# Optimization experiments

Hardware: AMD Instinct MI355X
Metric: run time of the kernel (lower is better)

## Reference

```python
import jax, jax.numpy as jnp
import numpy as np

NG, NL, NCAM, NP, ED = 8, 4, 6, 7, 256  # groups, levels, cams, key points, embed dims
GD = ED // NG
FIX_SCALE = jnp.array([[0.0, 0.0, 0.0], [0.45, 0.0, 0.0], [-0.45, 0.0, 0.0],
                       [0.0, 0.45, 0.0], [0.0, -0.45, 0.0], [0.0, 0.0, 0.45],
                       [0.0, 0.0, -0.45]], dtype=jnp.float32)


def grid_sample_bilinear(feat, grid):
    """feat [N,C,H,W], grid [N,A,P,2] in [-1,1]; bilinear, zeros padding, align_corners=False."""
    N, C, H, W = feat.shape
    A, P = grid.shape[1], grid.shape[2]
    gx = (grid[..., 0] + 1.0) * (W * 0.5) - 0.5
    gy = (grid[..., 1] + 1.0) * (H * 0.5) - 0.5
    x0 = jnp.floor(gx)
    y0 = jnp.floor(gy)
    wx1 = gx - x0
    wy1 = gy - y0
    feat_flat = feat.reshape(N, C, H * W)

    def gather(xi, yi, w):
        valid = (xi >= 0) & (xi <= W - 1) & (yi >= 0) & (yi <= H - 1)
        xc = jnp.clip(xi, 0, W - 1).astype(jnp.int32)
        yc = jnp.clip(yi, 0, H - 1).astype(jnp.int32)
        idx = (yc * W + xc).reshape(N, 1, A * P)
        vals = jnp.take_along_axis(feat_flat, idx, axis=2)  # [N,C,A*P]
        return vals * (w * valid).reshape(N, 1, A * P)

    out = (gather(x0, y0, (1.0 - wx1) * (1.0 - wy1))
           + gather(x0 + 1.0, y0, wx1 * (1.0 - wy1))
           + gather(x0, y0 + 1.0, (1.0 - wx1) * wy1)
           + gather(x0 + 1.0, y0 + 1.0, wx1 * wy1))
    return out.reshape(N, C, A, P)


def _forward(instance_feature, anchor, anchor_embed, feat0, feat1, feat2, feat3,
             projection_mat, image_wh, w_fc, b_fc, w_out, b_out):
    B, A = anchor.shape[:2]
    # --- key point generation (box_code_size=8: size + yaw rotation + translation) ---
    size = jnp.exp(anchor[..., 3:6])[:, :, None, :]           # [B,A,1,3]
    kp = FIX_SCALE * size                                      # [B,A,7,3]
    sin, cos = anchor[..., 6], anchor[..., 7]
    z = jnp.zeros_like(cos)
    o = jnp.ones_like(cos)
    rot = jnp.stack([jnp.stack([cos, -sin, z], -1),
                     jnp.stack([sin, cos, z], -1),
                     jnp.stack([z, z, o], -1)], -2)            # [B,A,3,3]
    kp = jnp.einsum('baij,bapj->bapi', rot, kp) + anchor[..., None, 0:3]

    # --- attention weights: softmax over cams*levels*pts per group ---
    feature = instance_feature + anchor_embed
    w = feature @ w_fc.T + b_fc                                # [B,A,NG*NCAM*NL*NP]
    w = jax.nn.softmax(w.reshape(B, A, NCAM * NL * NP, NG), axis=2)
    w = w.reshape(B, A, NCAM, NL, NP, NG)

    # --- project key points to normalized image coords ---
    pts = jnp.concatenate([kp, jnp.ones_like(kp[..., :1])], -1)  # [B,A,7,4]
    p2d = jnp.einsum('bcij,bapj->bcapi', projection_mat, pts)[..., :3]
    xy = p2d[..., :2] / jnp.maximum(p2d[..., 2:3], 1e-5)
    xy = xy / jnp.maximum(image_wh[:, :, None, None], 1e-5)
    grid = (xy * 2.0 - 1.0).reshape(B * NCAM, A, NP, 2)

    # --- multilevel bilinear sampling ---
    levels = [feat0, feat1, feat2, feat3]
    sampled = jnp.stack([grid_sample_bilinear(f.reshape((B * NCAM,) + f.shape[2:]), grid)
                         for f in levels], axis=1)             # [B*Ncam,NL,C,A,P]
    feats = sampled.reshape(B, NCAM, NL, ED, A, NP).transpose(0, 4, 1, 2, 5, 3)  # [B,A,Ncam,NL,P,C]
    feats = feats.reshape(B, A, NCAM, NL, NP, NG, GD)

    # --- weighted fusion over cams, levels, then sum over key points ---
    fused = jnp.einsum('bacnpgd,bacnpg->bagd', feats, w).reshape(B, A, ED)
    return fused @ w_out.T + b_out


def setup_inputs() -> dict:
    ks = jax.random.split(jax.random.key(0), 13)
    B, A = 2, 900
    return {
        'instance_feature': jax.random.normal(ks[0], (B, A, ED), jnp.float32),
        'anchor': jax.random.normal(ks[1], (B, A, 8), jnp.float32),
        'anchor_embed': jax.random.normal(ks[2], (B, A, ED), jnp.float32),
        'feat0': jax.random.normal(ks[3], (B, NCAM, ED, 64, 176), jnp.float32),
        'feat1': jax.random.normal(ks[4], (B, NCAM, ED, 32, 88), jnp.float32),
        'feat2': jax.random.normal(ks[5], (B, NCAM, ED, 16, 44), jnp.float32),
        'feat3': jax.random.normal(ks[6], (B, NCAM, ED, 8, 22), jnp.float32),
        'projection_mat': jax.random.normal(ks[7], (B, NCAM, 4, 4), jnp.float32),
        'image_wh': jnp.ones((B, NCAM, 2), jnp.float32),
        'w_fc': jax.random.normal(ks[8], (NG * NCAM * NL * NP, ED), jnp.float32) * 0.02,
        'b_fc': jax.random.normal(ks[9], (NG * NCAM * NL * NP,), jnp.float32) * 0.02,
        'w_out': jax.random.normal(ks[10], (ED, ED), jnp.float32) * 0.02,
        'b_out': jax.random.normal(ks[11], (ED,), jnp.float32) * 0.02,
    }


def reference(instance_feature, anchor, anchor_embed, feat0, feat1, feat2, feat3,
              projection_mat, image_wh, w_fc, b_fc, w_out, b_out):
    return _forward(instance_feature, anchor, anchor_embed, feat0, feat1, feat2, feat3,
                    projection_mat, image_wh, w_fc, b_fc, w_out, b_out)
```

## Files before the change

kernel.cpp:

```cpp
#include <hip/hip_runtime.h>
#include <math.h>

constexpr int B = 2, A = 900, ED = 256, NG = 8, NCAM = 6, NL = 4, NP = 7;
constexpr int NJ = NG * NCAM * NL * NP;
constexpr int NBA = B * A;
constexpr int NE = NCAM * NL * NP;

__constant__ float FIXS[NP][3] = {
  {0.f,0.f,0.f},{0.45f,0.f,0.f},{-0.45f,0.f,0.f},
  {0.f,0.45f,0.f},{0.f,-0.45f,0.f},{0.f,0.f,0.45f},{0.f,0.f,-0.45f}};

__constant__ int cH[NL]  = {64,32,16,8};
__constant__ int cW[NL]  = {176,88,44,22};
__constant__ int cHW[NL] = {11264,2816,704,176};

__global__ __launch_bounds__(256) void k_tr(const float* __restrict__ in,
                                            float* __restrict__ out, int R, int C)
{
  __shared__ float tile[32][33];
  const int r0 = blockIdx.y * 32, c0 = blockIdx.x * 32;
  const int tx = threadIdx.x, ty = threadIdx.y;
#pragma unroll
  for (int kk = 0; kk < 4; ++kk) {
    const int r = r0 + ty + kk*8, c = c0 + tx;
    if (r < R && c < C) tile[ty + kk*8][tx] = in[(size_t)r*C + c];
  }
  __syncthreads();
#pragma unroll
  for (int kk = 0; kk < 4; ++kk) {
    const int c = c0 + ty + kk*8, r = r0 + tx;
    if (r < R && c < C) out[(size_t)c*R + r] = tile[tx][ty + kk*8];
  }
}

__global__ __launch_bounds__(192) void k_fc(const float* __restrict__ inst,
    const float* __restrict__ emb, const float* __restrict__ wt,
    const float* __restrict__ b_fc, float* __restrict__ wraw)
{
  __shared__ float fsh[8][ED];
  const int a0 = blockIdx.x * 8;
  const int j  = blockIdx.y * 192 + threadIdx.x;
  const int t  = threadIdx.x;

  for (int i = t; i < 8 * ED; i += 192) {
    const int a = i >> 8, k = i & 255;
    const size_t idx = (size_t)(a0 + a) * ED + k;
    fsh[a][k] = inst[idx] + emb[idx];
  }
  __syncthreads();

  float acc[8] = {0.f,0.f,0.f,0.f,0.f,0.f,0.f,0.f};
  for (int k = 0; k < ED; k += 4) {
    float w0 = wt[(size_t)(k+0)*NJ + j];
    float w1 = wt[(size_t)(k+1)*NJ + j];
    float w2 = wt[(size_t)(k+2)*NJ + j];
    float w3 = wt[(size_t)(k+3)*NJ + j];
#pragma unroll
    for (int a = 0; a < 8; ++a)
      acc[a] += w0*fsh[a][k] + w1*fsh[a][k+1] + w2*fsh[a][k+2] + w3*fsh[a][k+3];
  }
  const float bj = b_fc[j];
#pragma unroll
  for (int a = 0; a < 8; ++a)
    wraw[(size_t)(a0+a)*NJ + j] = acc[a] + bj;
}

__global__ __launch_bounds__(256) void k_sample_g(
    const float* __restrict__ anchor, const float* __restrict__ proj,
    const float* __restrict__ wh, const float* __restrict__ wraw,
    const float* __restrict__ f0, const float* __restrict__ f1,
    const float* __restrict__ f2, const float* __restrict__ f3,
    float* __restrict__ fused)
{
  __shared__ float wsh[NJ];
  __shared__ float gridsh[NCAM][NP][2];
  __shared__ const float* cbase[NE];
  __shared__ float4 cwt[NE];
  __shared__ int4   cmeta[NE];
  __shared__ int wcnt[4];

  const int ba = blockIdx.x;
  const int b  = ba / A;
  const int t  = threadIdx.x;

  for (int j = t; j < NJ; j += 256) wsh[j] = wraw[(size_t)ba*NJ + j];

  if (t < NCAM*NP) {
    const int c = t / NP, p = t % NP;
    const float* an = anchor + (size_t)ba * 8;
    const float sx = expf(an[3]), sy = expf(an[4]), sz = expf(an[5]);
    const float sn = an[6], cs = an[7];
    const float kx = FIXS[p][0]*sx, ky = FIXS[p][1]*sy, kz = FIXS[p][2]*sz;
    const float px = cs*kx - sn*ky + an[0];
    const float py = sn*kx + cs*ky + an[1];
    const float pz = kz + an[2];
    const float* P = proj + ((size_t)(b*NCAM + c))*16;
    const float X = P[0]*px + P[1]*py + P[2]*pz  + P[3];
    const float Y = P[4]*px + P[5]*py + P[6]*pz  + P[7];
    const float Z = P[8]*px + P[9]*py + P[10]*pz + P[11];
    const float zc  = fmaxf(Z, 1e-5f);
    const float whx = fmaxf(wh[(b*NCAM+c)*2+0], 1e-5f);
    const float why = fmaxf(wh[(b*NCAM+c)*2+1], 1e-5f);
    gridsh[c][p][0] = (X/zc/whx)*2.f - 1.f;
    gridsh[c][p][1] = (Y/zc/why)*2.f - 1.f;
  }
  __syncthreads();

  bool valid = false;
  int fl = 0, Wl = 0, HWl = 0;
  float wx1 = 0.f, wy1 = 0.f;
  const float* bptr = nullptr;
  if (t < NE) {
    const int c = t / (NL*NP); const int r = t % (NL*NP);
    const int l = r / NP, p = r % NP;
    Wl = cW[l]; HWl = cHW[l];
    const int Hl = cH[l];
    const float gx = (gridsh[c][p][0] + 1.f) * (Wl * 0.5f) - 0.5f;
    const float gy = (gridsh[c][p][1] + 1.f) * (Hl * 0.5f) - 0.5f;
    const float x0f = floorf(gx), y0f = floorf(gy);
    const bool vx0 = (x0f >=  0.f) & (x0f <= (float)(Wl-1));
    const bool vx1 = (x0f >= -1.f) & (x0f <= (float)(Wl-2));
    const bool vy0 = (y0f >=  0.f) & (y0f <= (float)(Hl-1));
    const bool vy1 = (y0f >= -1.f) & (y0f <= (float)(Hl-2));
    fl = ((vx0&&vy0)?1:0) | ((vx1&&vy0)?2:0) | ((vx0&&vy1)?4:0) | ((vx1&&vy1)?8:0);
    if (fl) {
      wx1 = gx - x0f; wy1 = gy - y0f;
      const int x0 = (int)x0f, y0 = (int)y0f;
      const float* fp = (l==0) ? f0 : (l==1) ? f1 : (l==2) ? f2 : f3;
      bptr = fp + (size_t)(b*NCAM + c) * ED * HWl + (long long)(y0*Wl + x0);
      valid = true;
    }
  }

  const unsigned long long mask = __ballot(valid);
  const int lane = t & 63, wv = t >> 6;
  if (lane == 0) wcnt[wv] = __popcll(mask);
  __syncthreads();
  int off = 0, nv = 0;
#pragma unroll
  for (int i = 0; i < 4; ++i) { if (i < wv) off += wcnt[i]; nv += wcnt[i]; }
  if (valid) {
    const int pos = off + __popcll(mask & ((1ull << lane) - 1ull));
    cbase[pos] = bptr;
    cwt[pos]   = make_float4((1.f-wx1)*(1.f-wy1), wx1*(1.f-wy1),
                             (1.f-wx1)*wy1,       wx1*wy1);
    cmeta[pos] = make_int4(Wl, HWl, fl, t);
  }

  {
    const int g = t >> 5, ln = t & 31;
    float m = -3.4e38f;
    for (int i = ln; i < NE; i += 32) m = fmaxf(m, wsh[i*NG + g]);
#pragma unroll
    for (int mk = 16; mk >= 1; mk >>= 1) m = fmaxf(m, __shfl_xor(m, mk));
    float s = 0.f;
    for (int i = ln; i < NE; i += 32) {
      const float e = expf(wsh[i*NG + g] - m);
      wsh[i*NG + g] = e;
      s += e;
    }
#pragma unroll
    for (int mk = 16; mk >= 1; mk >>= 1) s += __shfl_xor(s, mk);
    const float inv = 1.f / s;
    for (int i = ln; i < NE; i += 32) wsh[i*NG + g] *= inv;
  }
  __syncthreads();

  float acc = 0.f;
  const int g = t >> 5;
  for (int i = 0; i < nv; ++i) {
    const float* bp = cbase[i];
    const float4 w4 = cwt[i];
    const int4 m = cmeta[i];
    const float* pb = bp + (long long)t * m.y;
    const float aw = wsh[m.w*NG + g];
    float sv = 0.f;
    const int f = m.z;
    if (f == 15) {
      sv = w4.x*pb[0] + w4.y*pb[1] + w4.z*pb[m.x] + w4.w*pb[m.x+1];
    } else {
      if (f & 1) sv += w4.x*pb[0];
      if (f & 2) sv += w4.y*pb[1];
      if (f & 4) sv += w4.z*pb[m.x];
      if (f & 8) sv += w4.w*pb[m.x+1];
    }
    acc += aw * sv;
  }
  fused[(size_t)ba*ED + t] = acc;
}

__global__ __launch_bounds__(256) void k_out(const float* __restrict__ fused,
    const float* __restrict__ w_out, const float* __restrict__ b_out,
    float* __restrict__ out)
{
  __shared__ float fsh[8][ED];
  const int a0 = blockIdx.x * 8;
  const int t = threadIdx.x;
#pragma unroll
  for (int k = 0; k < 8; ++k) fsh[k][t] = fused[(size_t)(a0+k)*ED + t];
  __syncthreads();
  float acc[8] = {0.f,0.f,0.f,0.f,0.f,0.f,0.f,0.f};
  for (int i = 0; i < ED; i += 4) {
    const float4 w4 = *(const float4*)&w_out[(size_t)t*ED + i];
#pragma unroll
    for (int k = 0; k < 8; ++k) {
      const float4 fv = *(const float4*)&fsh[k][i];
      acc[k] += w4.x*fv.x + w4.y*fv.y + w4.z*fv.z + w4.w*fv.w;
    }
  }
  const float bo = b_out[t];
#pragma unroll
  for (int k = 0; k < 8; ++k) out[(size_t)(a0+k)*ED + t] = acc[k] + bo;
}

extern "C" void kernel_launch(void* const* d_in, const int* in_sizes, int n_in,
                              void* d_out, int out_size, void* d_ws, size_t ws_size,
                              hipStream_t stream) {
  const float* inst   = (const float*)d_in[0];
  const float* anchor = (const float*)d_in[1];
  const float* emb    = (const float*)d_in[2];
  const float* f0 = (const float*)d_in[3];
  const float* f1 = (const float*)d_in[4];
  const float* f2 = (const float*)d_in[5];
  const float* f3 = (const float*)d_in[6];
  const float* proj  = (const float*)d_in[7];
  const float* wh    = (const float*)d_in[8];
  const float* w_fc  = (const float*)d_in[9];
  const float* b_fc  = (const float*)d_in[10];
  const float* w_out = (const float*)d_in[11];
  const float* b_out = (const float*)d_in[12];
  float* out = (float*)d_out;
  float* ws  = (float*)d_ws;

  const size_t WRAW  = (size_t)NBA * NJ;
  const size_t FUSED = (size_t)NBA * ED;
  float* wraw   = ws;
  float* fusedp = wraw + WRAW;
  float* wt     = fusedp + FUSED;

  k_tr<<<dim3(ED/32, NJ/32, 1), dim3(32,8), 0, stream>>>(w_fc, wt, NJ, ED);

  k_fc<<<dim3(NBA / 8, 7), 192, 0, stream>>>(inst, emb, wt, b_fc, wraw);

  k_sample_g<<<NBA, 256, 0, stream>>>(anchor, proj, wh, wraw,
                                      f0, f1, f2, f3, fusedp);

  k_out<<<NBA / 8, 256, 0, stream>>>(fusedp, w_out, b_out, out);
}
```

Baseline: 414.5 us.

## Transpose feature maps to channel-last before bilinear sampling for coalesced gathers

Adds a kernel that rewrites all four feature levels from CHW to HWC layout in workspace on every call. The sampling kernel can then read the 256 channels of each corner as one contiguous row instead of 256 loads strided by the plane size. This trades an extra full read and write of roughly 184 MB of feature data for far fewer scattered cache lines touched during the gather. The softmax weight buffer is also stored group-major. A fallback kernel that samples the native layout runs when the workspace is too small.

```diff
diff --git a/kernel.cpp b/kernel.cpp
--- a/kernel.cpp
+++ b/kernel.cpp
@@ -5,6 +5,7 @@
 constexpr int NJ = NG * NCAM * NL * NP;
 constexpr int NBA = B * A;
 constexpr int NE = NCAM * NL * NP;
+constexpr int LDST = 260;
 
 __constant__ float FIXS[NP][3] = {
   {0.f,0.f,0.f},{0.45f,0.f,0.f},{-0.45f,0.f,0.f},
@@ -13,6 +14,47 @@
 __constant__ int cH[NL]  = {64,32,16,8};
 __constant__ int cW[NL]  = {176,88,44,22};
 __constant__ int cHW[NL] = {11264,2816,704,176};
+__constant__ long long cLOFF[NL] = {0LL, 34603008LL, 43253760LL, 45416448LL};
+
+__global__ __launch_bounds__(256) void k_tr_cl(
+    const float* __restrict__ f0, const float* __restrict__ f1,
+    const float* __restrict__ f2, const float* __restrict__ f3,
+    float* __restrict__ tfeat)
+{
+  __shared__ float tile[32 * LDST];
+  const int bc = blockIdx.y;
+  const int bx = blockIdx.x;
+  int lvl, t0;
+  if      (bx < 352) { lvl = 0; t0 = 0; }
+  else if (bx < 440) { lvl = 1; t0 = 352; }
+  else if (bx < 462) { lvl = 2; t0 = 440; }
+  else               { lvl = 3; t0 = 462; }
+  const int HW  = cHW[lvl];
+  const int px0 = (bx - t0) * 32;
+  const float* in = ((lvl==0)?f0:(lvl==1)?f1:(lvl==2)?f2:f3)
+                    + (size_t)bc * ED * HW + px0;
+  float* outp = tfeat + cLOFF[lvl] + ((size_t)bc * HW + px0) * ED;
+  const int t = threadIdx.x;
+  const int npx = min(32, HW - px0);
+
+#pragma unroll
+  for (int j = 0; j < 8; ++j) {
+    const int px = 4 * j;
+    if (px < npx) {
+      const float4 v = *(const float4*)(in + (size_t)t * HW + px);
+      tile[(px+0)*LDST + t] = v.x;
+      tile[(px+1)*LDST + t] = v.y;
+      tile[(px+2)*LDST + t] = v.z;
+      tile[(px+3)*LDST + t] = v.w;
+    }
+  }
+  __syncthreads();
+  const int wv = t >> 6, l = t & 63;
+  for (int px = wv; px < npx; px += 4) {
+    const float4 v = *(const float4*)&tile[px*LDST + 4*l];
+    *(float4*)(outp + (size_t)px * ED + 4*l) = v;
+  }
+}
 
 __global__ __launch_bounds__(256) void k_tr(const float* __restrict__ in,
                                             float* __restrict__ out, int R, int C)
@@ -65,12 +107,10 @@
     wraw[(size_t)(a0+a)*NJ + j] = acc[a] + bj;
 }
 
-__global__ __launch_bounds__(256) void k_sample_g(
+__global__ __launch_bounds__(256) void k_sample_cl(
     const float* __restrict__ anchor, const float* __restrict__ proj,
     const float* __restrict__ wh, const float* __restrict__ wraw,
-    const float* __restrict__ f0, const float* __restrict__ f1,
-    const float* __restrict__ f2, const float* __restrict__ f3,
-    float* __restrict__ fused)
+    const float* __restrict__ tfeat, float* __restrict__ fused)
 {
   __shared__ float wsh[NJ];
   __shared__ float gridsh[NCAM][NP][2];
@@ -83,7 +123,8 @@
   const int b  = ba / A;
   const int t  = threadIdx.x;
 
-  for (int j = t; j < NJ; j += 256) wsh[j] = wraw[(size_t)ba*NJ + j];
+  for (int j = t; j < NJ; j += 256)
+    wsh[(j & 7) * NE + (j >> 3)] = wraw[(size_t)ba*NJ + j];
 
   if (t < NCAM*NP) {
     const int c = t / NP, p = t % NP;
@@ -107,14 +148,13 @@
   __syncthreads();
 
   bool valid = false;
-  int fl = 0, Wl = 0, HWl = 0;
+  int fl = 0, rowoff = 0;
   float wx1 = 0.f, wy1 = 0.f;
   const float* bptr = nullptr;
   if (t < NE) {
     const int c = t / (NL*NP); const int r = t % (NL*NP);
     const int l = r / NP, p = r % NP;
-    Wl = cW[l]; HWl = cHW[l];
-    const int Hl = cH[l];
+    const int Wl = cW[l], Hl = cH[l], HWl = cHW[l];
     const float gx = (gridsh[c][p][0] + 1.f) * (Wl * 0.5f) - 0.5f;
     const float gy = (gridsh[c][p][1] + 1.f) * (Hl * 0.5f) - 0.5f;
     const float x0f = floorf(gx), y0f = floorf(gy);
@@ -126,8 +166,9 @@
     if (fl) {
       wx1 = gx - x0f; wy1 = gy - y0f;
       const int x0 = (int)x0f, y0 = (int)y0f;
-      const float* fp = (l==0) ? f0 : (l==1) ? f1 : (l==2) ? f2 : f3;
-      bptr = fp + (size_t)(b*NCAM + c) * ED * HWl + (long long)(y0*Wl + x0);
+      bptr = tfeat + cLOFF[l]
+           + ((size_t)(b*NCAM + c) * HWl + (long long)(y0*Wl + x0)) * ED;
+      rowoff = Wl * ED;
       valid = true;
     }
   }
@@ -144,47 +185,126 @@
     cbase[pos] = bptr;
     cwt[pos]   = make_float4((1.f-wx1)*(1.f-wy1), wx1*(1.f-wy1),
                              (1.f-wx1)*wy1,       wx1*wy1);
-    cmeta[pos] = make_int4(Wl, HWl, fl, t);
+    cmeta[pos] = make_int4(rowoff, fl, t, 0);
   }
 
   {
     const int g = t >> 5, ln = t & 31;
+    float* wg = wsh + g * NE;
     float m = -3.4e38f;
-    for (int i = ln; i < NE; i += 32) m = fmaxf(m, wsh[i*NG + g]);
+    for (int i = ln; i < NE; i += 32) m = fmaxf(m, wg[i]);
 #pragma unroll
     for (int mk = 16; mk >= 1; mk >>= 1) m = fmaxf(m, __shfl_xor(m, mk));
     float s = 0.f;
     for (int i = ln; i < NE; i += 32) {
-      const float e = expf(wsh[i*NG + g] - m);
-      wsh[i*NG + g] = e;
+      const float e = expf(wg[i] - m);
+      wg[i] = e;
       s += e;
     }
 #pragma unroll
     for (int mk = 16; mk >= 1; mk >>= 1) s += __shfl_xor(s, mk);
     const float inv = 1.f / s;
-    for (int i = ln; i < NE; i += 32) wsh[i*NG + g] *= inv;
+    for (int i = ln; i < NE; i += 32) wg[i] *= inv;
   }
   __syncthreads();
 
   float acc = 0.f;
   const int g = t >> 5;
   for (int i = 0; i < nv; ++i) {
-    const float* bp = cbase[i];
+    const float* pb = cbase[i] + t;
     const float4 w4 = cwt[i];
     const int4 m = cmeta[i];
-    const float* pb = bp + (long long)t * m.y;
-    const float aw = wsh[m.w*NG + g];
+    const float aw = wsh[g*NE + m.z];
+    const int ro = m.x, f = m.y;
     float sv = 0.f;
-    const int f = m.z;
     if (f == 15) {
-      sv = w4.x*pb[0] + w4.y*pb[1] + w4.z*pb[m.x] + w4.w*pb[m.x+1];
+      sv = w4.x*pb[0] + w4.y*pb[ED] + w4.z*pb[ro] + w4.w*pb[ro+ED];
     } else {
       if (f & 1) sv += w4.x*pb[0];
-      if (f & 2) sv += w4.y*pb[1];
-      if (f & 4) sv += w4.z*pb[m.x];
-      if (f & 8) sv += w4.w*pb[m.x+1];
+      if (f & 2) sv += w4.y*pb[ED];
+      if (f & 4) sv += w4.z*pb[ro];
+      if (f & 8) sv += w4.w*pb[ro+ED];
     }
     acc += aw * sv;
+  }
+  fused[(size_t)ba*ED + t] = acc;
+}
+
+__global__ __launch_bounds__(256) void k_sample_nat(
+    const float* __restrict__ anchor, const float* __restrict__ proj,
+    const float* __restrict__ wh, const float* __restrict__ wraw,
+    const float* __restrict__ f0, const float* __restrict__ f1,
+    const float* __restrict__ f2, const float* __restrict__ f3,
+    float* __restrict__ fused)
+{
+  __shared__ float wsh[NJ];
+  __shared__ float gridsh[NCAM][NP][2];
+  const int ba = blockIdx.x;
+  const int b  = ba / A;
+  const int t  = threadIdx.x;
+  for (int j = t; j < NJ; j += 256)
+    wsh[(j & 7) * NE + (j >> 3)] = wraw[(size_t)ba*NJ + j];
+  if (t < NCAM*NP) {
+    const int c = t / NP, p = t % NP;
+    const float* an = anchor + (size_t)ba * 8;
+    const float sx = expf(an[3]), sy = expf(an[4]), sz = expf(an[5]);
+    const float sn = an[6], cs = an[7];
+    const float kx = FIXS[p][0]*sx, ky = FIXS[p][1]*sy, kz = FIXS[p][2]*sz;
+    const float px = cs*kx - sn*ky + an[0];
+    const float py = sn*kx + cs*ky + an[1];
+    const float pz = kz + an[2];
+    const float* P = proj + ((size_t)(b*NCAM + c))*16;
+    const float X = P[0]*px + P[1]*py + P[2]*pz  + P[3];
+    const float Y = P[4]*px + P[5]*py + P[6]*pz  + P[7];
+    const float Z = P[8]*px + P[9]*py + P[10]*pz + P[11];
+    const float zc  = fmaxf(Z, 1e-5f);
+    const float whx = fmaxf(wh[(b*NCAM+c)*2+0], 1e-5f);
+    const float why = fmaxf(wh[(b*NCAM+c)*2+1], 1e-5f);
+    gridsh[c][p][0] = (X/zc/whx)*2.f - 1.f;
+    gridsh[c][p][1] = (Y/zc/why)*2.f - 1.f;
+  }
+  __syncthreads();
+  {
+    const int g = t >> 5, ln = t & 31;
+    float* wg = wsh + g * NE;
+    float m = -3.4e38f;
+    for (int i = ln; i < NE; i += 32) m = fmaxf(m, wg[i]);
+#pragma unroll
+    for (int mk = 16; mk >= 1; mk >>= 1) m = fmaxf(m, __shfl_xor(m, mk));
+    float s = 0.f;
+    for (int i = ln; i < NE; i += 32) { const float e = expf(wg[i]-m); wg[i]=e; s+=e; }
+#pragma unroll
+    for (int mk = 16; mk >= 1; mk >>= 1) s += __shfl_xor(s, mk);
+    const float inv = 1.f / s;
+    for (int i = ln; i < NE; i += 32) wg[i] *= inv;
+  }
+  __syncthreads();
+  float acc = 0.f;
+  const int g = t >> 5;
+  for (int e = 0; e < NE; ++e) {
+    const int c = e / (NL*NP);
+    const int l = (e / NP) % NL;
+    const int p = e % NP;
+    const int Wl = cW[l], Hl = cH[l], HWl = cHW[l];
+    const float gx = (gridsh[c][p][0] + 1.f) * (Wl * 0.5f) - 0.5f;
+    const float gy = (gridsh[c][p][1] + 1.f) * (Hl * 0.5f) - 0.5f;
+    const float x0f = floorf(gx), y0f = floorf(gy);
+    const bool vx0 = (x0f >=  0.f) & (x0f <= (float)(Wl-1));
+    const bool vx1 = (x0f >= -1.f) & (x0f <= (float)(Wl-2));
+    const bool vy0 = (y0f >=  0.f) & (y0f <= (float)(Hl-1));
+    const bool vy1 = (y0f >= -1.f) & (y0f <= (float)(Hl-2));
+    const int fl = ((vx0&&vy0)?1:0)|((vx1&&vy0)?2:0)|((vx0&&vy1)?4:0)|((vx1&&vy1)?8:0);
+    if (!fl) continue;
+    const float wx1 = gx - x0f, wy1 = gy - y0f;
+    const int x0 = (int)x0f, y0 = (int)y0f;
+    const float* fp = (l==0)?f0:(l==1)?f1:(l==2)?f2:f3;
+    const float* pb = fp + ((size_t)(b*NCAM+c)*ED + t)*HWl + (long long)(y0*Wl+x0);
+    float sv = 0.f;
+    if (fl & 1) sv += (1.f-wx1)*(1.f-wy1)*pb[0];
+    if (fl & 2) sv += wx1*(1.f-wy1)*pb[1];
+    if (fl & 4) sv += (1.f-wx1)*wy1*pb[Wl];
+    if (fl & 8) sv += wx1*wy1*pb[Wl+1];
+    acc += wsh[g*NE + e] * sv;
   }
   fused[(size_t)ba*ED + t] = acc;
 }
@@ -232,18 +352,29 @@
   float* out = (float*)d_out;
   float* ws  = (float*)d_ws;
 
+  const size_t TFEAT = 45957120ULL;
   const size_t WRAW  = (size_t)NBA * NJ;
   const size_t FUSED = (size_t)NBA * ED;
-  float* wraw   = ws;
+  const size_t WT    = (size_t)ED * NJ;
+  const bool tr = ws_size >= (TFEAT + WRAW + FUSED + WT) * sizeof(float);
+
+  float* tfeat  = ws;
+  float* wraw   = tr ? (ws + TFEAT) : ws;
   float* fusedp = wraw + WRAW;
   float* wt     = fusedp + FUSED;
 
   k_tr<<<dim3(ED/32, NJ/32, 1), dim3(32,8), 0, stream>>>(w_fc, wt, NJ, ED);
 
+  if (tr)
+    k_tr_cl<<<dim3(468, B*NCAM), 256, 0, stream>>>(f0, f1, f2, f3, tfeat);
+
   k_fc<<<dim3(NBA / 8, 7), 192, 0, stream>>>(inst, emb, wt, b_fc, wraw);
 
-  k_sample_g<<<NBA, 256, 0, stream>>>(anchor, proj, wh, wraw,
-                                      f0, f1, f2, f3, fusedp);
+  if (tr)
+    k_sample_cl<<<NBA, 256, 0, stream>>>(anchor, proj, wh, wraw, tfeat, fusedp);
+  else
+    k_sample_nat<<<NBA, 256, 0, stream>>>(anchor, proj, wh, wraw,
+                                          f0, f1, f2, f3, fusedp);
 
   k_out<<<NBA / 8, 256, 0, stream>>>(fusedp, w_out, b_out, out);
 }
```

Measured after the change: 424.9 us. 2.5% more time.

## Transpose levels 1-3 feature maps to channels-last for coalesced bilinear gathers

Applied to the files above, without the earlier changes.

Adds a kernel that rewrites feature levels 1-3 from channel-major to pixel-major (channels-last) layout in workspace. The sampler then reads 256 consecutive channels per corner, so its gathers become coalesced instead of strided by the plane size. Level 0 is left in its original layout, probably to avoid transposing the largest map. The attention-weight shared buffer is also re-laid out group-major to avoid strided shared accesses. The cost is an extra full pass over levels 1-3 on every call, plus extra workspace, and the new path is used only when the workspace is large enough.

```diff
diff --git a/kernel.cpp b/kernel.cpp
--- a/kernel.cpp
+++ b/kernel.cpp
@@ -5,6 +5,7 @@
 constexpr int NJ = NG * NCAM * NL * NP;
 constexpr int NBA = B * A;
 constexpr int NE = NCAM * NL * NP;
+constexpr int LDST = 260;
 
 __constant__ float FIXS[NP][3] = {
   {0.f,0.f,0.f},{0.45f,0.f,0.f},{-0.45f,0.f,0.f},
@@ -13,6 +14,44 @@
 __constant__ int cH[NL]  = {64,32,16,8};
 __constant__ int cW[NL]  = {176,88,44,22};
 __constant__ int cHW[NL] = {11264,2816,704,176};
+__constant__ long long cLOFF[NL] = {0LL, 0LL, 8650752LL, 10813440LL};
+
+__global__ __launch_bounds__(256) void k_tr_cl(
+    const float* __restrict__ f1, const float* __restrict__ f2,
+    const float* __restrict__ f3, float* __restrict__ tfeat)
+{
+  __shared__ float tile[32 * LDST];
+  const int bc = blockIdx.y;
+  const int bx = blockIdx.x;
+  int lvl, t0;
+  if      (bx < 88)  { lvl = 1; t0 = 0; }
+  else if (bx < 110) { lvl = 2; t0 = 88; }
+  else               { lvl = 3; t0 = 110; }
+  const int HW  = cHW[lvl];
+  const int px0 = (bx - t0) * 32;
+  const float* in = ((lvl==1)?f1:(lvl==2)?f2:f3) + (size_t)bc * ED * HW + px0;
+  float* outp = tfeat + cLOFF[lvl] + ((size_t)bc * HW + px0) * ED;
+  const int t = threadIdx.x;
+  const int npx = min(32, HW - px0);
+
+#pragma unroll
+  for (int j = 0; j < 8; ++j) {
+    const int px = 4 * j;
+    if (px < npx) {
+      const float4 v = *(const float4*)(in + (size_t)t * HW + px);
+      tile[(px+0)*LDST + t] = v.x;
+      tile[(px+1)*LDST + t] = v.y;
+      tile[(px+2)*LDST + t] = v.z;
+      tile[(px+3)*LDST + t] = v.w;
+    }
+  }
+  __syncthreads();
+  const int wv = t >> 6, l = t & 63;
+  for (int px = wv; px < npx; px += 4) {
+    const float4 v = *(const float4*)&tile[px*LDST + 4*l];
+    *(float4*)(outp + (size_t)px * ED + 4*l) = v;
+  }
+}
 
 __global__ __launch_bounds__(256) void k_tr(const float* __restrict__ in,
                                             float* __restrict__ out, int R, int C)
@@ -65,9 +104,11 @@
     wraw[(size_t)(a0+a)*NJ + j] = acc[a] + bj;
 }
 
-__global__ __launch_bounds__(256) void k_sample_g(
+template<bool CL>
+__global__ __launch_bounds__(256) void k_sample_h(
     const float* __restrict__ anchor, const float* __restrict__ proj,
     const float* __restrict__ wh, const float* __restrict__ wraw,
+    const float* __restrict__ tfeat,
     const float* __restrict__ f0, const float* __restrict__ f1,
     const float* __restrict__ f2, const float* __restrict__ f3,
     float* __restrict__ fused)
@@ -83,7 +124,8 @@
   const int b  = ba / A;
   const int t  = threadIdx.x;
 
-  for (int j = t; j < NJ; j += 256) wsh[j] = wraw[(size_t)ba*NJ + j];
+  for (int j = t; j < NJ; j += 256)
+    wsh[(j & 7) * NE + (j >> 3)] = wraw[(size_t)ba*NJ + j];
 
   if (t < NCAM*NP) {
     const int c = t / NP, p = t % NP;
@@ -107,14 +149,13 @@
   __syncthreads();
 
   bool valid = false;
-  int fl = 0, Wl = 0, HWl = 0;
+  int fl = 0, dx = 0, dy = 0, chstep = 0;
   float wx1 = 0.f, wy1 = 0.f;
   const float* bptr = nullptr;
   if (t < NE) {
     const int c = t / (NL*NP); const int r = t % (NL*NP);
     const int l = r / NP, p = r % NP;
-    Wl = cW[l]; HWl = cHW[l];
-    const int Hl = cH[l];
+    const int Wl = cW[l], Hl = cH[l], HWl = cHW[l];
     const float gx = (gridsh[c][p][0] + 1.f) * (Wl * 0.5f) - 0.5f;
     const float gy = (gridsh[c][p][1] + 1.f) * (Hl * 0.5f) - 0.5f;
     const float x0f = floorf(gx), y0f = floorf(gy);
@@ -126,8 +167,15 @@
     if (fl) {
       wx1 = gx - x0f; wy1 = gy - y0f;
       const int x0 = (int)x0f, y0 = (int)y0f;
-      const float* fp = (l==0) ? f0 : (l==1) ? f1 : (l==2) ? f2 : f3;
-      bptr = fp + (size_t)(b*NCAM + c) * ED * HWl + (long long)(y0*Wl + x0);
+      if (CL && l >= 1) {
+        bptr = tfeat + cLOFF[l]
+             + ((size_t)(b*NCAM + c) * HWl + (long long)(y0*Wl + x0)) * ED;
+        chstep = 1; dx = ED; dy = Wl * ED;
+      } else {
+        const float* fp = (l==0)?f0:(l==1)?f1:(l==2)?f2:f3;
+        bptr = fp + (size_t)(b*NCAM + c) * ED * HWl + (long long)(y0*Wl + x0);
+        chstep = HWl; dx = 1; dy = Wl;
+      }
       valid = true;
     }
   }
@@ -144,45 +192,45 @@
     cbase[pos] = bptr;
     cwt[pos]   = make_float4((1.f-wx1)*(1.f-wy1), wx1*(1.f-wy1),
                              (1.f-wx1)*wy1,       wx1*wy1);
-    cmeta[pos] = make_int4(Wl, HWl, fl, t);
+    cmeta[pos] = make_int4(dx, dy, fl | (t << 8), chstep);
   }
 
   {
     const int g = t >> 5, ln = t & 31;
+    float* wg = wsh + g * NE;
     float m = -3.4e38f;
-    for (int i = ln; i < NE; i += 32) m = fmaxf(m, wsh[i*NG + g]);
+    for (int i = ln; i < NE; i += 32) m = fmaxf(m, wg[i]);
 #pragma unroll
     for (int mk = 16; mk >= 1; mk >>= 1) m = fmaxf(m, __shfl_xor(m, mk));
     float s = 0.f;
     for (int i = ln; i < NE; i += 32) {
-      const float e = expf(wsh[i*NG + g] - m);
-      wsh[i*NG + g] = e;
+      const float e = expf(wg[i] - m);
+      wg[i] = e;
       s += e;
     }
 #pragma unroll
     for (int mk = 16; mk >= 1; mk >>= 1) s += __shfl_xor(s, mk);
     const float inv = 1.f / s;
-    for (int i = ln; i < NE; i += 32) wsh[i*NG + g] *= inv;
+    for (int i = ln; i < NE; i += 32) wg[i] *= inv;
   }
   __syncthreads();
 
   float acc = 0.f;
   const int g = t >> 5;
   for (int i = 0; i < nv; ++i) {
-    const float* bp = cbase[i];
+    const int4 m = cmeta[i];
+    const float* pb = cbase[i] + (size_t)t * m.w;
     const float4 w4 = cwt[i];
-    const int4 m = cmeta[i];
-    const float* pb = bp + (long long)t * m.y;
-    const float aw = wsh[m.w*NG + g];
+    const float aw = wsh[g*NE + (m.z >> 8)];
+    const int f = m.z & 255;
     float sv = 0.f;
-    const int f = m.z;
     if (f == 15) {
-      sv = w4.x*pb[0] + w4.y*pb[1] + w4.z*pb[m.x] + w4.w*pb[m.x+1];
+      sv = w4.x*pb[0] + w4.y*pb[m.x] + w4.z*pb[m.y] + w4.w*pb[m.x+m.y];
     } else {
       if (f & 1) sv += w4.x*pb[0];
-      if (f & 2) sv += w4.y*pb[1];
-      if (f & 4) sv += w4.z*pb[m.x];
-      if (f & 8) sv += w4.w*pb[m.x+1];
+      if (f & 2) sv += w4.y*pb[m.x];
+      if (f & 4) sv += w4.z*pb[m.y];
+      if (f & 8) sv += w4.w*pb[m.x+m.y];
     }
     acc += aw * sv;
   }
@@ -232,18 +280,30 @@
   float* out = (float*)d_out;
   float* ws  = (float*)d_ws;
 
+  const size_t TFEAT = 11354112ULL;
   const size_t WRAW  = (size_t)NBA * NJ;
   const size_t FUSED = (size_t)NBA * ED;
-  float* wraw   = ws;
+  const size_t WT    = (size_t)ED * NJ;
+  const bool tr = ws_size >= (TFEAT + WRAW + FUSED + WT) * sizeof(float);
+
+  float* tfeat  = ws;
+  float* wraw   = tr ? (ws + TFEAT) : ws;
   float* fusedp = wraw + WRAW;
   float* wt     = fusedp + FUSED;
 
   k_tr<<<dim3(ED/32, NJ/32, 1), dim3(32,8), 0, stream>>>(w_fc, wt, NJ, ED);
 
+  if (tr)
+    k_tr_cl<<<dim3(116, B*NCAM), 256, 0, stream>>>(f1, f2, f3, tfeat);
+
   k_fc<<<dim3(NBA / 8, 7), 192, 0, stream>>>(inst, emb, wt, b_fc, wraw);
 
-  k_sample_g<<<NBA, 256, 0, stream>>>(anchor, proj, wh, wraw,
-                                      f0, f1, f2, f3, fusedp);
+  if (tr)
+    k_sample_h<true><<<NBA, 256, 0, stream>>>(anchor, proj, wh, wraw, tfeat,
+                                              f0, f1, f2, f3, fusedp);
+  else
+    k_sample_h<false><<<NBA, 256, 0, stream>>>(anchor, proj, wh, wraw, tfeat,
+                                               f0, f1, f2, f3, fusedp);
 
   k_out<<<NBA / 8, 256, 0, stream>>>(fusedp, w_out, b_out, out);
 }
```

New measurement: 380.8 us. 1.09x faster.
